# Kernel tuning notes

Hardware: AMD Instinct MI355X
Metric: run time of the kernel (lower is better)

The kernel has to match this reference:

```python
import jax, jax.numpy as jnp
import numpy as np

NEG = -10000.0

def _wn(W, g):
    # weight_norm with dim=None: single scalar g scaling W / ||W||_F
    return g * W / jnp.linalg.norm(W)

def setup_inputs() -> dict:
    key = jax.random.key(0)
    ks = jax.random.split(key, 10)
    B, N, H, P = 128, 4096, 128, 128
    v = jax.random.normal(ks[0], (B, N, H), jnp.float32)
    q = jax.random.normal(ks[1], (B, H), jnp.float32)
    mask = jnp.ones((B, N), jnp.float32)
    # params (out_dim, in_dim) like torch Linear
    Wv = jax.random.normal(ks[2], (P, H), jnp.float32) / np.sqrt(H)
    bv = jnp.zeros((P,), jnp.float32)
    gv = jnp.float32(jnp.linalg.norm(Wv))
    Wq = jax.random.normal(ks[3], (P, H), jnp.float32) / np.sqrt(H)
    bq = jnp.zeros((P,), jnp.float32)
    gq = jnp.float32(jnp.linalg.norm(Wq))
    Wa = jax.random.normal(ks[4], (1, P), jnp.float32) / np.sqrt(P)
    ba = jnp.zeros((1,), jnp.float32)
    ga = jnp.float32(jnp.linalg.norm(Wa))
    return {"v": v, "q": q, "mask": mask, "Wv": Wv, "bv": bv, "gv": gv,
            "Wq": Wq, "bq": bq, "gq": gq, "Wa": Wa, "ba": ba, "ga": ga}

def reference(v, q, mask, Wv, bv, gv, Wq, bq, gq, Wa, ba, ga):
    # FCNet projections (dropout is identity at inference; FCNet applies no relu)
    v_proj = jnp.einsum('bnh,ph->bnp', v, _wn(Wv, gv)) + bv        # [B,N,P]
    q_proj = (q @ _wn(Wq, gq).T + bq)[:, None, :]                   # [B,1,P]
    h = jax.nn.relu(v_proj + q_proj)                                # [B,N,P]
    logits = jnp.einsum('bnp,p->bn', h, _wn(Wa, ga)[0]) + ba[0]     # [B,N]
    logits = logits + (1.0 - mask) * NEG
    w = jax.nn.softmax(logits, axis=-1)                             # [B,N]
    w_att = w[:, :, None]                                           # [B,N,1]
    att = jnp.sum(v * w_att, axis=1)                                # [B,H]
    return att, w_att
```

## Files before the change

kernel.cpp:

```cpp
#include <hip/hip_runtime.h>

typedef _Float16 half8_t __attribute__((ext_vector_type(8)));
typedef float f32x4 __attribute__((ext_vector_type(4)));

#define B_ 128
#define N_ 4096
#define H_ 128
#define P_ 128
#define CCH 8
#define ROWS_PER_CHUNK (N_ / CCH)
#define TILES (ROWS_PER_CHUNK / 64)

#define OFF_SCALES 0
#define OFF_WA     16
#define OFF_QPC    256
#define OFF_BPACK  16640
#define OFF_LOGITS 24832
#define OFF_PART   549120
#define OFF_FIN    819456

__device__ __forceinline__ float block_reduce_sum(float val, float* red, int tid) {
    red[tid] = val;
    __syncthreads();
    for (int s = 128; s > 0; s >>= 1) {
        if (tid < s) red[tid] += red[tid + s];
        __syncthreads();
    }
    float r = red[0];
    __syncthreads();
    return r;
}

__global__ __launch_bounds__(256) void k0a_prep(
    const float* __restrict__ Wv, const float* __restrict__ gv,
    const float* __restrict__ Wq, const float* __restrict__ gq,
    const float* __restrict__ Wa, const float* __restrict__ ga,
    float* __restrict__ ws)
{
    __shared__ float red[256];
    __shared__ float s_sv, s_sa;
    const int tid = threadIdx.x;

    float sv2 = 0.f, sq2 = 0.f, sa2 = 0.f;
    for (int i = tid; i < P_ * H_; i += 256) {
        float x = Wv[i]; sv2 += x * x;
        float y = Wq[i]; sq2 += y * y;
    }
    if (tid < P_) { float z = Wa[tid]; sa2 = z * z; }

    float nv2 = block_reduce_sum(sv2, red, tid);
    float nq2 = block_reduce_sum(sq2, red, tid);
    float na2 = block_reduce_sum(sa2, red, tid);

    if (tid == 0) {
        float sv = gv[0] / sqrtf(nv2);
        float sq = gq[0] / sqrtf(nq2);
        float sa = ga[0] / sqrtf(na2);
        ws[OFF_SCALES + 0] = sv;
        ws[OFF_SCALES + 1] = sq;
        ws[OFF_SCALES + 2] = sa;
        s_sv = sv; s_sa = sa;
    }
    __syncthreads();

    const float sv = s_sv, sa = s_sa;
    _Float16* bp = (_Float16*)(ws + OFF_BPACK);
    for (int s = tid; s < 16384; s += 256) {
        int j  = s & 7;
        int L  = (s >> 3) & 63;
        int pt = (s >> 9) & 7;
        int kk = s >> 12;
        int p = pt * 16 + (L & 15);
        int h = kk * 32 + (L >> 4) * 8 + j;
        bp[s] = (_Float16)(Wv[p * H_ + h] * sv);
    }
    if (tid < P_) ws[OFF_WA + tid] = Wa[tid] * sa;
}

__global__ __launch_bounds__(128) void k0b_qproj(
    const float* __restrict__ q, const float* __restrict__ Wq,
    const float* __restrict__ bq, const float* __restrict__ bv,
    float* __restrict__ ws)
{
    const int b = blockIdx.x, p = threadIdx.x;
    const float sq = ws[OFF_SCALES + 1];
    const float* qr = q + b * H_;
    const float* wr = Wq + p * H_;
    float acc = 0.f;
#pragma unroll 8
    for (int h = 0; h < H_; ++h) acc += qr[h] * wr[h];
    ws[OFF_QPC + b * P_ + p] = acc * sq + bq[p] + bv[p];
}

__global__ __launch_bounds__(256) void k1_main(
    const float* __restrict__ v, const float* __restrict__ mask,
    const float* __restrict__ ba, float* __restrict__ ws)
{
    const int c = blockIdx.x;
    const int b = blockIdx.y;
    const int tid = threadIdx.x;
    const int lane = tid & 63;
    const int w = tid >> 6;

    __shared__ __align__(16) _Float16 Bl[16384];
    __shared__ float qpcs[P_];
    __shared__ float was[P_];
    __shared__ float smask[ROWS_PER_CHUNK];
    __shared__ float obuf[4][P_];
    __shared__ float mbuf[4], lbuf[4];

    {
        const uint4* src = (const uint4*)(ws + OFF_BPACK);
        uint4* dst = (uint4*)Bl;
#pragma unroll
        for (int i = 0; i < 8; ++i) dst[tid + i * 256] = src[tid + i * 256];
        if (tid < P_) {
            qpcs[tid] = ws[OFF_QPC + b * P_ + tid];
            was[tid]  = ws[OFF_WA + tid];
        }
#pragma unroll
        for (int i = 0; i < ROWS_PER_CHUNK / 256; ++i)
            smask[tid + i * 256] = mask[(size_t)b * N_ + c * ROWS_PER_CHUNK + tid + i * 256];
    }
    const float ba0 = ba[0];
    __syncthreads();

    const int rloc = lane & 15;
    const int grp  = lane >> 4;
    const int colb = grp * 8;

    float m_w = -1e30f, l_w = 0.f;
    float o32[32];
#pragma unroll
    for (int j = 0; j < 32; ++j) o32[j] = 0.f;

    for (int it = 0; it < TILES; ++it) {
        const int r0 = it * 64 + w * 16;
        const int n0w = c * ROWS_PER_CHUNK + r0;

        const float* vrow = v + ((size_t)b * N_ + n0w + rloc) * H_;
        half8_t af[4];
#pragma unroll
        for (int kk = 0; kk < 4; ++kk) {
            const float4* p4 = (const float4*)(vrow + kk * 32 + colb);
            float4 f0 = p4[0], f1 = p4[1];
            half8_t a;
            a[0] = (_Float16)f0.x; a[1] = (_Float16)f0.y;
            a[2] = (_Float16)f0.z; a[3] = (_Float16)f0.w;
            a[4] = (_Float16)f1.x; a[5] = (_Float16)f1.y;
            a[6] = (_Float16)f1.z; a[7] = (_Float16)f1.w;
            af[kk] = a;
        }

        float lp[4];
        lp[0] = lp[1] = lp[2] = lp[3] = 0.f;
#pragma unroll
        for (int pt = 0; pt < 8; ++pt) {
            const int p = pt * 16 + rloc;
            const float qv = qpcs[p];
            f32x4 acc = {qv, qv, qv, qv};
#pragma unroll
            for (int kk = 0; kk < 4; ++kk) {
                half8_t bf = *(const half8_t*)&Bl[(((kk * 8 + pt) * 64) + lane) * 8];
                acc = __builtin_amdgcn_mfma_f32_16x16x32_f16(af[kk], bf, acc, 0, 0, 0);
            }
            const float wv = was[p];
#pragma unroll
            for (int r = 0; r < 4; ++r)
                lp[r] += fmaxf(acc[r], 0.f) * wv;
        }
#pragma unroll
        for (int m = 1; m <= 8; m <<= 1) {
#pragma unroll
            for (int r = 0; r < 4; ++r) lp[r] += __shfl_xor(lp[r], m, 64);
        }
#pragma unroll
        for (int r = 0; r < 4; ++r) {
            const float mk = smask[r0 + grp * 4 + r];
            lp[r] += ba0 + (1.0f - mk) * (-10000.0f);
        }

        const int srcl = (rloc >> 2) << 4;
        float t0 = __shfl(lp[0], srcl, 64);
        float t1 = __shfl(lp[1], srcl, 64);
        float t2 = __shfl(lp[2], srcl, 64);
        float t3 = __shfl(lp[3], srcl, 64);
        float a01 = (rloc & 1) ? t1 : t0;
        float a23 = (rloc & 1) ? t3 : t2;
        float lg_me = (rloc & 2) ? a23 : a01;

        if (lane < 16) ws[OFF_LOGITS + (size_t)b * N_ + n0w + lane] = lg_me;

        float mt = fmaxf(fmaxf(lp[0], lp[1]), fmaxf(lp[2], lp[3]));
        mt = fmaxf(mt, __shfl_xor(mt, 16, 64));
        mt = fmaxf(mt, __shfl_xor(mt, 32, 64));

        const float mn = fmaxf(m_w, mt);
        const float alpha = __expf(m_w - mn);
        const float wme = __expf(lg_me - mn);
        float s = wme;
#pragma unroll
        for (int m = 1; m <= 8; m <<= 1) s += __shfl_xor(s, m, 64);
        l_w = l_w * alpha + s;
        m_w = mn;

        if (alpha != 1.0f) {
#pragma unroll
            for (int j = 0; j < 32; ++j) o32[j] *= alpha;
        }
#pragma unroll
        for (int kk = 0; kk < 4; ++kk) {
#pragma unroll
            for (int j = 0; j < 8; ++j)
                o32[kk * 8 + j] += wme * (float)af[kk][j];
        }
    }

#pragma unroll
    for (int m = 1; m <= 8; m <<= 1) {
#pragma unroll
        for (int j = 0; j < 32; ++j) o32[j] += __shfl_xor(o32[j], m, 64);
    }
    {
        const int j0 = rloc * 2;
#pragma unroll
        for (int u = 0; u < 2; ++u) {
            const int j = j0 + u;
            obuf[w][(j >> 3) * 32 + colb + (j & 7)] = o32[j];
        }
        if (lane == 0) { mbuf[w] = m_w; lbuf[w] = l_w; }
    }
    __syncthreads();

    float* part = ws + OFF_PART + ((size_t)b * CCH + c) * 132;
    if (tid < P_) {
        const float mb = fmaxf(fmaxf(mbuf[0], mbuf[1]), fmaxf(mbuf[2], mbuf[3]));
        float lb = 0.f, oh = 0.f;
#pragma unroll
        for (int ww = 0; ww < 4; ++ww) {
            const float e = __expf(mbuf[ww] - mb);
            lb += e * lbuf[ww];
            oh += e * obuf[ww][tid];
        }
        part[2 + tid] = oh;
        if (tid == 0) { part[0] = mb; part[1] = lb; }
    }
}

__global__ __launch_bounds__(128) void k2a_combine(
    float* __restrict__ ws, float* __restrict__ out)
{
    const int b = blockIdx.x, h = threadIdx.x;
    const float* part = ws + OFF_PART + (size_t)b * CCH * 132;
    float m = -1e30f;
#pragma unroll
    for (int c = 0; c < CCH; ++c) m = fmaxf(m, part[c * 132]);
    float l = 0.f, a = 0.f;
#pragma unroll
    for (int c = 0; c < CCH; ++c) {
        const float e = __expf(part[c * 132] - m);
        l += e * part[c * 132 + 1];
        a += e * part[c * 132 + 2 + h];
    }
    out[b * H_ + h] = a / l;
    if (h == 0) {
        ws[OFF_FIN + b] = m;
        ws[OFF_FIN + B_ + b] = 1.0f / l;
    }
}

__global__ __launch_bounds__(256) void k2b_weights(
    const float* __restrict__ ws, float* __restrict__ out)
{
    const int idx = blockIdx.x * 256 + threadIdx.x;
    const int b = idx >> 12;
    const float lg = ws[OFF_LOGITS + idx];
    out[B_ * H_ + idx] = __expf(lg - ws[OFF_FIN + b]) * ws[OFF_FIN + B_ + b];
}

extern "C" void kernel_launch(void* const* d_in, const int* in_sizes, int n_in,
                              void* d_out, int out_size, void* d_ws, size_t ws_size,
                              hipStream_t stream) {
    const float* v    = (const float*)d_in[0];
    const float* q    = (const float*)d_in[1];
    const float* mask = (const float*)d_in[2];
    const float* Wv   = (const float*)d_in[3];
    const float* bv   = (const float*)d_in[4];
    const float* gv   = (const float*)d_in[5];
    const float* Wq   = (const float*)d_in[6];
    const float* bq   = (const float*)d_in[7];
    const float* gq   = (const float*)d_in[8];
    const float* Wa   = (const float*)d_in[9];
    const float* ba   = (const float*)d_in[10];
    const float* ga   = (const float*)d_in[11];
    float* out = (float*)d_out;
    float* ws  = (float*)d_ws;

    k0a_prep<<<1, 256, 0, stream>>>(Wv, gv, Wq, gq, Wa, ga, ws);
    k0b_qproj<<<B_, 128, 0, stream>>>(q, Wq, bq, bv, ws);
    k1_main<<<dim3(CCH, B_), 256, 0, stream>>>(v, mask, ba, ws);
    k2a_combine<<<B_, 128, 0, stream>>>(ws, out);
    k2b_weights<<<(B_ * N_) / 256, 256, 0, stream>>>(ws, out);
}
```

Baseline: 434.3 us.

## Use 1024-thread blocks over fewer chunks and register-prefetch next v tile

The main kernel now launches 16 waves per block over 2 chunks per batch instead of 4 waves over 8 chunks, so fewer blocks each reload the packed weight matrix into LDS. It also software-prefetches the next tile of v rows into registers while the current tile runs through MFMA, overlapping global loads with compute. In exchange, 1024-thread blocks with 32 accumulators plus 8 prefetch float4s per thread put heavy pressure on registers. The grid also shrinks to 256 blocks, which may underfill the GPU.

```diff
diff --git a/kernel.cpp b/kernel.cpp
--- a/kernel.cpp
+++ b/kernel.cpp
@@ -7,9 +7,10 @@
 #define N_ 4096
 #define H_ 128
 #define P_ 128
-#define CCH 8
+#define CCH 2
 #define ROWS_PER_CHUNK (N_ / CCH)
-#define TILES (ROWS_PER_CHUNK / 64)
+#define NWAVE 16
+#define TILES (ROWS_PER_CHUNK / (NWAVE * 16))
 
 #define OFF_SCALES 0
 #define OFF_WA     16
@@ -92,7 +93,7 @@
     ws[OFF_QPC + b * P_ + p] = acc * sq + bq[p] + bv[p];
 }
 
-__global__ __launch_bounds__(256) void k1_main(
+__global__ __launch_bounds__(1024) void k1_main(
     const float* __restrict__ v, const float* __restrict__ mask,
     const float* __restrict__ ba, float* __restrict__ ws)
 {
@@ -106,21 +107,21 @@
     __shared__ float qpcs[P_];
     __shared__ float was[P_];
     __shared__ float smask[ROWS_PER_CHUNK];
-    __shared__ float obuf[4][P_];
-    __shared__ float mbuf[4], lbuf[4];
+    __shared__ float obuf[NWAVE][P_];
+    __shared__ float mbuf[NWAVE], lbuf[NWAVE];
 
     {
         const uint4* src = (const uint4*)(ws + OFF_BPACK);
         uint4* dst = (uint4*)Bl;
 #pragma unroll
-        for (int i = 0; i < 8; ++i) dst[tid + i * 256] = src[tid + i * 256];
+        for (int i = 0; i < 2; ++i) dst[tid + i * 1024] = src[tid + i * 1024];
         if (tid < P_) {
             qpcs[tid] = ws[OFF_QPC + b * P_ + tid];
             was[tid]  = ws[OFF_WA + tid];
         }
 #pragma unroll
-        for (int i = 0; i < ROWS_PER_CHUNK / 256; ++i)
-            smask[tid + i * 256] = mask[(size_t)b * N_ + c * ROWS_PER_CHUNK + tid + i * 256];
+        for (int i = 0; i < ROWS_PER_CHUNK / 1024; ++i)
+            smask[tid + i * 1024] = mask[(size_t)b * N_ + c * ROWS_PER_CHUNK + tid + i * 1024];
     }
     const float ba0 = ba[0];
     __syncthreads();
@@ -134,22 +135,40 @@
 #pragma unroll
     for (int j = 0; j < 32; ++j) o32[j] = 0.f;
 
+    const float* vrow0 = v + ((size_t)b * N_ + c * ROWS_PER_CHUNK + w * 16 + rloc) * H_ + colb;
+
+    float4 pf[8];
+#pragma unroll
+    for (int kk = 0; kk < 4; ++kk) {
+        const float4* p4 = (const float4*)(vrow0 + kk * 32);
+        pf[2 * kk]     = p4[0];
+        pf[2 * kk + 1] = p4[1];
+    }
+
     for (int it = 0; it < TILES; ++it) {
-        const int r0 = it * 64 + w * 16;
+        const int r0 = it * (NWAVE * 16) + w * 16;
         const int n0w = c * ROWS_PER_CHUNK + r0;
 
-        const float* vrow = v + ((size_t)b * N_ + n0w + rloc) * H_;
         half8_t af[4];
 #pragma unroll
         for (int kk = 0; kk < 4; ++kk) {
-            const float4* p4 = (const float4*)(vrow + kk * 32 + colb);
-            float4 f0 = p4[0], f1 = p4[1];
+            float4 f0 = pf[2 * kk], f1 = pf[2 * kk + 1];
             half8_t a;
             a[0] = (_Float16)f0.x; a[1] = (_Float16)f0.y;
             a[2] = (_Float16)f0.z; a[3] = (_Float16)f0.w;
             a[4] = (_Float16)f1.x; a[5] = (_Float16)f1.y;
             a[6] = (_Float16)f1.z; a[7] = (_Float16)f1.w;
             af[kk] = a;
+        }
+
+        if (it + 1 < TILES) {
+            const float* vn = vrow0 + (size_t)(it + 1) * (NWAVE * 16) * H_;
+#pragma unroll
+            for (int kk = 0; kk < 4; ++kk) {
+                const float4* p4 = (const float4*)(vn + kk * 32);
+                pf[2 * kk]     = p4[0];
+                pf[2 * kk + 1] = p4[1];
+            }
         }
 
         float lp[4];
@@ -234,10 +253,12 @@
 
     float* part = ws + OFF_PART + ((size_t)b * CCH + c) * 132;
     if (tid < P_) {
-        const float mb = fmaxf(fmaxf(mbuf[0], mbuf[1]), fmaxf(mbuf[2], mbuf[3]));
+        float mb = -1e30f;
+#pragma unroll
+        for (int ww = 0; ww < NWAVE; ++ww) mb = fmaxf(mb, mbuf[ww]);
         float lb = 0.f, oh = 0.f;
 #pragma unroll
-        for (int ww = 0; ww < 4; ++ww) {
+        for (int ww = 0; ww < NWAVE; ++ww) {
             const float e = __expf(mbuf[ww] - mb);
             lb += e * lbuf[ww];
             oh += e * obuf[ww][tid];
@@ -298,7 +319,7 @@
 
     k0a_prep<<<1, 256, 0, stream>>>(Wv, gv, Wq, gq, Wa, ga, ws);
     k0b_qproj<<<B_, 128, 0, stream>>>(q, Wq, bq, bv, ws);
-    k1_main<<<dim3(CCH, B_), 256, 0, stream>>>(v, mask, ba, ws);
+    k1_main<<<dim3(CCH, B_), 1024, 0, stream>>>(v, mask, ba, ws);
     k2a_combine<<<B_, 128, 0, stream>>>(ws, out);
     k2b_weights<<<(B_ * N_) / 256, 256, 0, stream>>>(ws, out);
 }
```

Result: slower. 608.2 us (+40.1%).
